# Kernel optimization log

Measured on AMD Instinct MI355X. Metric: run time of the kernel, lower is better.

Reference implementation:

```python
import jax, jax.numpy as jnp
import numpy as np

TOP_K = 2
NOISE_STD = 1.0
EPS = 1e-9

def setup_inputs() -> dict:
    key = jax.random.key(0)
    k1, k2, k3, k4 = jax.random.split(key, 4)
    B, S, H, E = 4, 4096, 4096, 64
    hidden_states = jax.random.normal(k1, (B, S, H), dtype=jnp.float32)
    noise = jax.random.normal(k2, (B, S, E), dtype=jnp.float32)
    lim = 1.0 / np.sqrt(H)  # torch Linear default init scale
    w_gate = jax.random.uniform(k3, (E, H), dtype=jnp.float32, minval=-lim, maxval=lim)
    w_noise = jax.random.uniform(k4, (E, H), dtype=jnp.float32, minval=-lim, maxval=lim)
    return {"hidden_states": hidden_states, "noise": noise, "w_gate": w_gate, "w_noise": w_noise}

def reference(hidden_states, noise, w_gate, w_noise):
    # Gate and noise projections: [B,S,H] x [E,H]^T -> [B,S,E]
    router_logits = jnp.einsum('bsh,eh->bse', hidden_states, w_gate)
    noise_scale = jax.nn.softplus(jnp.einsum('bsh,eh->bse', hidden_states, w_noise))
    router_logits = router_logits + noise * noise_scale * NOISE_STD
    router_probs = jax.nn.softmax(router_logits, axis=-1)
    top_k_weights, top_k_indices = jax.lax.top_k(router_probs, TOP_K)
    top_k_weights = top_k_weights / (jnp.sum(top_k_weights, axis=-1, keepdims=True) + EPS)
    # Scatter normalized weights back to dense [B,S,E] via one-hot (E is small)
    E = router_probs.shape[-1]
    gate_weights = jnp.sum(jax.nn.one_hot(top_k_indices, E, dtype=router_probs.dtype) * top_k_weights[..., None], axis=-2)
    return gate_weights, top_k_indices, router_logits
```

## Files before the change

kernel.cpp:

```cpp
#include <hip/hip_runtime.h>
#include <math.h>


typedef float   f32x4   __attribute__((ext_vector_type(4)));
typedef __bf16  bf16x8  __attribute__((ext_vector_type(8)));
typedef unsigned short ushort8 __attribute__((ext_vector_type(8)));

#define EE 64
#define E2 128
#define NT 8
#define BM 64

__device__ __forceinline__ unsigned short bf16_rne(float f) {
    unsigned int u = __float_as_uint(f);
    u += 0x7fffu + ((u >> 16) & 1u);
    return (unsigned short)(u >> 16);
}
__device__ __forceinline__ float bf16_f32(unsigned short h) {
    return __uint_as_float(((unsigned int)h) << 16);
}
__device__ __forceinline__ void split3(float a, unsigned short& h1,
                                       unsigned short& h2, unsigned short& h3) {
    h1 = bf16_rne(a);
    float r  = a - bf16_f32(h1);
    h2 = bf16_rne(r);
    float r2 = r - bf16_f32(h2);
    h3 = bf16_rne(r2);
}

__device__ __forceinline__ void gload_lds16(const void* g, void* l) {
    __builtin_amdgcn_global_load_lds(
        (const __attribute__((address_space(1))) void*)g,
        (__attribute__((address_space(3))) void*)l, 16, 0, 0);
}

__global__ __launch_bounds__(256) void pack_b(
    const float* __restrict__ wg, const float* __restrict__ wn,
    unsigned short* __restrict__ bp, int Hdim)
{
    int pair = blockIdx.x * 4 + (threadIdx.x >> 6);
    int l    = threadIdx.x & 63;
    int ks   = pair >> 3;
    int nt   = pair & 7;
    int col  = nt * 16 + (l & 15);
    int k    = ks * 32 + ((l >> 4) * 8);
    const float* wrow = (col < EE) ? (wg + (size_t)col * Hdim)
                                   : (wn + (size_t)(col - EE) * Hdim);
    float4 v0 = *reinterpret_cast<const float4*>(wrow + k);
    float4 v1 = *reinterpret_cast<const float4*>(wrow + k + 4);
    float vals[8] = {v0.x, v0.y, v0.z, v0.w, v1.x, v1.y, v1.z, v1.w};
    ushort8 t1, t2, t3;
    #pragma unroll
    for (int j = 0; j < 8; ++j) {
        unsigned short a, b, c;
        split3(vals[j], a, b, c);
        t1[j] = a; t2[j] = b; t3[j] = c;
    }
    size_t base = ((size_t)(ks * 8 + nt) * 3) * 512 + (size_t)l * 8;
    *reinterpret_cast<ushort8*>(bp + base        ) = t1;
    *reinterpret_cast<ushort8*>(bp + base + 512  ) = t2;
    *reinterpret_cast<ushort8*>(bp + base + 1024 ) = t3;
}

#define MFMA(a, b, c) __builtin_amdgcn_mfma_f32_16x16x32_bf16((a), (b), (c), 0, 0, 0)

__global__ __launch_bounds__(512, 2) void router_mfma(
    const float* __restrict__ hs,
    const float* __restrict__ noise,
    const unsigned short* __restrict__ bp,
    float* __restrict__ out_gate,
    float* __restrict__ out_idx,
    float* __restrict__ out_logits,
    int Ntok, int Hdim)
{
    __shared__ unsigned short Bst[2][2][24 * 512];
    __shared__ float Lred[BM][E2 + 5];

    const int tid  = threadIdx.x;
    const int lane = tid & 63;
    const int w    = tid >> 6;
    const int kh   = w >> 2;
    const int mi   = w & 3;
    const int m0   = blockIdx.x * BM;

    const int khalf = Hdim >> 1;
    const int steps = khalf >> 5;

    f32x4 acc[NT];
    #pragma unroll
    for (int nt = 0; nt < NT; ++nt) acc[nt] = f32x4{0.f, 0.f, 0.f, 0.f};

    const float* pa = hs + (size_t)(m0 + mi * 16 + (lane & 15)) * Hdim
                         + (size_t)kh * khalf + ((lane >> 4) * 8);

    const unsigned short* srcB[6];
    unsigned short* dstB[2][6];
    #pragma unroll
    for (int j = 0; j < 6; ++j) {
        int c   = tid + 512 * j;
        int ckh = c / 1536;
        int r   = c % 1536;
        int f   = r >> 6;
        int l   = r & 63;
        srcB[j]    = bp + (size_t)(ckh * steps) * 12288 + f * 512 + l * 8;
        dstB[0][j] = &Bst[0][ckh][f * 512 + l * 8];
        dstB[1][j] = &Bst[1][ckh][f * 512 + l * 8];
    }

    #define STAGE(buf)                                                        \
        do {                                                                  \
            _Pragma("unroll")                                                 \
            for (int j = 0; j < 6; ++j) {                                     \
                gload_lds16(srcB[j], dstB[buf][j]);                           \
                srcB[j] += 12288;                                             \
            }                                                                 \
        } while (0)

    #define LOADA(d0, d1)                                                     \
        do {                                                                  \
            d0 = *reinterpret_cast<const float4*>(pa);                        \
            d1 = *reinterpret_cast<const float4*>(pa + 4);                    \
            pa += 32;                                                         \
        } while (0)

    #define COMPUTE(s0, s1, buf)                                              \
        do {                                                                  \
            float vals[8] = {s0.x, s0.y, s0.z, s0.w, s1.x, s1.y, s1.z, s1.w}; \
            bf16x8 A1, A2, A3;                                                \
            _Pragma("unroll")                                                 \
            for (int j = 0; j < 8; ++j) {                                     \
                float a  = vals[j];                                           \
                __bf16 h1 = (__bf16)a;                                        \
                float r  = a - (float)h1;                                     \
                __bf16 h2 = (__bf16)r;                                        \
                float r2 = r - (float)h2;                                     \
                __bf16 h3 = (__bf16)r2;                                       \
                A1[j] = h1; A2[j] = h2; A3[j] = h3;                           \
            }                                                                 \
            const unsigned short* bb = &Bst[buf][kh][lane * 8];               \
            ushort8 bf[24];                                                   \
            _Pragma("unroll")                                                 \
            for (int f = 0; f < 24; ++f)                                      \
                bf[f] = *reinterpret_cast<const ushort8*>(bb + f * 512);      \
            _Pragma("unroll")                                                 \
            for (int nt = 0; nt < NT; ++nt) {                                 \
                bf16x8 b1 = __builtin_bit_cast(bf16x8, bf[nt * 3 + 0]);       \
                bf16x8 b2 = __builtin_bit_cast(bf16x8, bf[nt * 3 + 1]);       \
                bf16x8 b3 = __builtin_bit_cast(bf16x8, bf[nt * 3 + 2]);       \
                f32x4 c = acc[nt];                                            \
                c = MFMA(A1, b1, c);                                          \
                c = MFMA(A1, b2, c);                                          \
                c = MFMA(A2, b1, c);                                          \
                c = MFMA(A2, b2, c);                                          \
                c = MFMA(A1, b3, c);                                          \
                c = MFMA(A3, b1, c);                                          \
                acc[nt] = c;                                                  \
            }                                                                 \
        } while (0)

    STAGE(0);
    float4 c0, c1, n0, n1;
    LOADA(c0, c1);
    __syncthreads();

    for (int s = 0; s < steps; s += 2) {
        STAGE(1);
        LOADA(n0, n1);
        COMPUTE(c0, c1, 0);
        __syncthreads();
        if (s + 2 < steps) {
            STAGE(0);
            LOADA(c0, c1);
        }
        COMPUTE(n0, n1, 1);
        __syncthreads();
    }

    if (kh == 0) {
        #pragma unroll
        for (int nt = 0; nt < NT; ++nt)
            #pragma unroll
            for (int r = 0; r < 4; ++r)
                Lred[mi * 16 + (lane >> 4) * 4 + r][nt * 16 + (lane & 15)] = acc[nt][r];
    }
    __syncthreads();
    if (kh == 1) {
        #pragma unroll
        for (int nt = 0; nt < NT; ++nt)
            #pragma unroll
            for (int r = 0; r < 4; ++r)
                Lred[mi * 16 + (lane >> 4) * 4 + r][nt * 16 + (lane & 15)] += acc[nt][r];
    }
    __syncthreads();

    if (tid < BM) {
        const int t   = tid;
        const int tok = m0 + t;
        const float* nrow = noise + (size_t)tok * EE;
        float* lrow = out_logits + (size_t)tok * EE;

        float m = -3.4e38f;
        for (int e = 0; e < EE; ++e) {
            float gv = Lred[t][e];
            float nv = Lred[t][EE + e];
            float sp = fmaxf(nv, 0.f) + log1pf(expf(-fabsf(nv)));
            float l  = fmaf(nrow[e], sp, gv);
            lrow[e]  = l;
            Lred[t][e] = l;
            m = fmaxf(m, l);
        }

        float Z = 0.f;
        float p1 = -1.f, p2 = -1.f;
        int   i1 = 0,    i2 = 0;
        for (int e = 0; e < EE; ++e) {
            float p = expf(Lred[t][e] - m);
            Z += p;
            if (p > p1)      { p2 = p1; i2 = i1; p1 = p; i1 = e; }
            else if (p > p2) { p2 = p;  i2 = e; }
        }
        float q1 = p1 / Z, q2 = p2 / Z;
        float denom = q1 + q2 + 1e-9f;
        float w1 = q1 / denom, w2 = q2 / denom;

        out_idx[(size_t)tok * 2 + 0] = (float)i1;
        out_idx[(size_t)tok * 2 + 1] = (float)i2;

        float* grow = out_gate + (size_t)tok * EE;
        for (int e = 0; e < EE; ++e)
            grow[e] = (e == i1) ? w1 : ((e == i2) ? w2 : 0.f);
    }
}

extern "C" void kernel_launch(void* const* d_in, const int* in_sizes, int n_in,
                              void* d_out, int out_size, void* d_ws, size_t ws_size,
                              hipStream_t stream) {
    const float* hs    = (const float*)d_in[0];
    const float* noise = (const float*)d_in[1];
    const float* wg    = (const float*)d_in[2];
    const float* wn    = (const float*)d_in[3];

    const int Ntok = in_sizes[1] / EE;
    const int Hdim = in_sizes[2] / EE;

    float* out_gate   = (float*)d_out;
    float* out_idx    = out_gate + (size_t)Ntok * EE;
    float* out_logits = out_idx  + (size_t)Ntok * 2;

    unsigned short* bp = (unsigned short*)d_ws;

    int pairs = (Hdim / 32) * 8;
    hipLaunchKernelGGL(pack_b, dim3(pairs / 4), dim3(256), 0, stream, wg, wn, bp, Hdim);

    hipLaunchKernelGGL(router_mfma, dim3(Ntok / BM), dim3(512), 0, stream,
                       hs, noise, bp, out_gate, out_idx, out_logits, Ntok, Hdim);
}
```

Before: 161.8 us.

## Split expert columns across waves instead of K halves, shrink block tile

Changes the work split inside a block: rather than two K-halves each computing all 128 output columns for 64 rows, the block now takes 32 rows and each of 8 waves owns 16 rows by 32 columns across the full K range. This removes the cross-wave K reduction, cuts accumulator registers and LDS (Bst and Lred now share a union), and raises the occupancy target to 4 blocks per CU. It also wraps the MFMA sequence in s_setprio. The cost is that each wave now converts its A tile into three bf16 parts for a quarter of the MFMA work, so the split overhead per MFMA goes up, and since each block covers half as many rows, the B operand gets less reuse per LDS load.

Result: slower. 241.5 us (+49.2%).

```diff
diff --git a/kernel.cpp b/kernel.cpp
--- a/kernel.cpp
+++ b/kernel.cpp
@@ -8,8 +8,7 @@
 
 #define EE 64
 #define E2 128
-#define NT 8
-#define BM 64
+#define BM 32
 
 __device__ __forceinline__ unsigned short bf16_rne(float f) {
     unsigned int u = __float_as_uint(f);
@@ -64,7 +63,12 @@
 
 #define MFMA(a, b, c) __builtin_amdgcn_mfma_f32_16x16x32_bf16((a), (b), (c), 0, 0, 0)
 
-__global__ __launch_bounds__(512, 2) void router_mfma(
+union ShMem {
+    unsigned short Bst[2][24 * 512];
+    float Lred[BM][E2 + 5];
+};
+
+__global__ __launch_bounds__(512, 4) void router_mfma(
     const float* __restrict__ hs,
     const float* __restrict__ noise,
     const unsigned short* __restrict__ bp,
@@ -73,44 +77,39 @@
     float* __restrict__ out_logits,
     int Ntok, int Hdim)
 {
-    __shared__ unsigned short Bst[2][2][24 * 512];
-    __shared__ float Lred[BM][E2 + 5];
+    __shared__ ShMem sh;
 
     const int tid  = threadIdx.x;
     const int lane = tid & 63;
     const int w    = tid >> 6;
-    const int kh   = w >> 2;
-    const int mi   = w & 3;
+    const int mi   = w & 1;
+    const int nq   = w >> 1;
     const int m0   = blockIdx.x * BM;
 
-    const int khalf = Hdim >> 1;
-    const int steps = khalf >> 5;
-
-    f32x4 acc[NT];
+    const int steps = Hdim >> 5;
+
+    f32x4 acc0 = f32x4{0.f, 0.f, 0.f, 0.f};
+    f32x4 acc1 = f32x4{0.f, 0.f, 0.f, 0.f};
+
+    const float* pa = hs + (size_t)(m0 + mi * 16 + (lane & 15)) * Hdim
+                         + ((lane >> 4) * 8);
+
+    const unsigned short* srcB[3];
+    unsigned short* dstB[2][3];
     #pragma unroll
-    for (int nt = 0; nt < NT; ++nt) acc[nt] = f32x4{0.f, 0.f, 0.f, 0.f};
-
-    const float* pa = hs + (size_t)(m0 + mi * 16 + (lane & 15)) * Hdim
-                         + (size_t)kh * khalf + ((lane >> 4) * 8);
-
-    const unsigned short* srcB[6];
-    unsigned short* dstB[2][6];
-    #pragma unroll
-    for (int j = 0; j < 6; ++j) {
-        int c   = tid + 512 * j;
-        int ckh = c / 1536;
-        int r   = c % 1536;
-        int f   = r >> 6;
-        int l   = r & 63;
-        srcB[j]    = bp + (size_t)(ckh * steps) * 12288 + f * 512 + l * 8;
-        dstB[0][j] = &Bst[0][ckh][f * 512 + l * 8];
-        dstB[1][j] = &Bst[1][ckh][f * 512 + l * 8];
+    for (int j = 0; j < 3; ++j) {
+        int c = tid + 512 * j;
+        int f = c >> 6;
+        int l = c & 63;
+        srcB[j]    = bp + (size_t)f * 512 + l * 8;
+        dstB[0][j] = &sh.Bst[0][f * 512 + l * 8];
+        dstB[1][j] = &sh.Bst[1][f * 512 + l * 8];
     }
 
     #define STAGE(buf)                                                        \
         do {                                                                  \
             _Pragma("unroll")                                                 \
-            for (int j = 0; j < 6; ++j) {                                     \
+            for (int j = 0; j < 3; ++j) {                                     \
                 gload_lds16(srcB[j], dstB[buf][j]);                           \
                 srcB[j] += 12288;                                             \
             }                                                                 \
@@ -137,25 +136,27 @@
                 __bf16 h3 = (__bf16)r2;                                       \
                 A1[j] = h1; A2[j] = h2; A3[j] = h3;                           \
             }                                                                 \
-            const unsigned short* bb = &Bst[buf][kh][lane * 8];               \
-            ushort8 bf[24];                                                   \
-            _Pragma("unroll")                                                 \
-            for (int f = 0; f < 24; ++f)                                      \
-                bf[f] = *reinterpret_cast<const ushort8*>(bb + f * 512);      \
-            _Pragma("unroll")                                                 \
-            for (int nt = 0; nt < NT; ++nt) {                                 \
-                bf16x8 b1 = __builtin_bit_cast(bf16x8, bf[nt * 3 + 0]);       \
-                bf16x8 b2 = __builtin_bit_cast(bf16x8, bf[nt * 3 + 1]);       \
-                bf16x8 b3 = __builtin_bit_cast(bf16x8, bf[nt * 3 + 2]);       \
-                f32x4 c = acc[nt];                                            \
-                c = MFMA(A1, b1, c);                                          \
-                c = MFMA(A1, b2, c);                                          \
-                c = MFMA(A2, b1, c);                                          \
-                c = MFMA(A2, b2, c);                                          \
-                c = MFMA(A1, b3, c);                                          \
-                c = MFMA(A3, b1, c);                                          \
-                acc[nt] = c;                                                  \
-            }                                                                 \
+            const unsigned short* bb = &sh.Bst[buf][lane * 8];                \
+            bf16x8 b10 = __builtin_bit_cast(bf16x8, *reinterpret_cast<const ushort8*>(bb + (nq * 6 + 0) * 512)); \
+            bf16x8 b20 = __builtin_bit_cast(bf16x8, *reinterpret_cast<const ushort8*>(bb + (nq * 6 + 1) * 512)); \
+            bf16x8 b30 = __builtin_bit_cast(bf16x8, *reinterpret_cast<const ushort8*>(bb + (nq * 6 + 2) * 512)); \
+            bf16x8 b11 = __builtin_bit_cast(bf16x8, *reinterpret_cast<const ushort8*>(bb + (nq * 6 + 3) * 512)); \
+            bf16x8 b21 = __builtin_bit_cast(bf16x8, *reinterpret_cast<const ushort8*>(bb + (nq * 6 + 4) * 512)); \
+            bf16x8 b31 = __builtin_bit_cast(bf16x8, *reinterpret_cast<const ushort8*>(bb + (nq * 6 + 5) * 512)); \
+            __builtin_amdgcn_s_setprio(1);                                    \
+            acc0 = MFMA(A1, b10, acc0);                                       \
+            acc0 = MFMA(A1, b20, acc0);                                       \
+            acc0 = MFMA(A2, b10, acc0);                                       \
+            acc0 = MFMA(A2, b20, acc0);                                       \
+            acc0 = MFMA(A1, b30, acc0);                                       \
+            acc0 = MFMA(A3, b10, acc0);                                       \
+            acc1 = MFMA(A1, b11, acc1);                                       \
+            acc1 = MFMA(A1, b21, acc1);                                       \
+            acc1 = MFMA(A2, b11, acc1);                                       \
+            acc1 = MFMA(A2, b21, acc1);                                       \
+            acc1 = MFMA(A1, b31, acc1);                                       \
+            acc1 = MFMA(A3, b11, acc1);                                       \
+            __builtin_amdgcn_s_setprio(0);                                    \
         } while (0)
 
     STAGE(0);
@@ -176,20 +177,14 @@
         __syncthreads();
     }
 
-    if (kh == 0) {
+    {
+        int row = mi * 16 + (lane >> 4) * 4;
+        int col = nq * 32 + (lane & 15);
         #pragma unroll
-        for (int nt = 0; nt < NT; ++nt)
-            #pragma unroll
-            for (int r = 0; r < 4; ++r)
-                Lred[mi * 16 + (lane >> 4) * 4 + r][nt * 16 + (lane & 15)] = acc[nt][r];
-    }
-    __syncthreads();
-    if (kh == 1) {
-        #pragma unroll
-        for (int nt = 0; nt < NT; ++nt)
-            #pragma unroll
-            for (int r = 0; r < 4; ++r)
-                Lred[mi * 16 + (lane >> 4) * 4 + r][nt * 16 + (lane & 15)] += acc[nt][r];
+        for (int r = 0; r < 4; ++r) {
+            sh.Lred[row + r][col]      = acc0[r];
+            sh.Lred[row + r][col + 16] = acc1[r];
+        }
     }
     __syncthreads();
 
@@ -201,12 +196,12 @@
 
         float m = -3.4e38f;
         for (int e = 0; e < EE; ++e) {
-            float gv = Lred[t][e];
-            float nv = Lred[t][EE + e];
+            float gv = sh.Lred[t][e];
+            float nv = sh.Lred[t][EE + e];
             float sp = fmaxf(nv, 0.f) + log1pf(expf(-fabsf(nv)));
             float l  = fmaf(nrow[e], sp, gv);
             lrow[e]  = l;
-            Lred[t][e] = l;
+            sh.Lred[t][e] = l;
             m = fmaxf(m, l);
         }
 
@@ -214,7 +209,7 @@
         float p1 = -1.f, p2 = -1.f;
         int   i1 = 0,    i2 = 0;
         for (int e = 0; e < EE; ++e) {
-            float p = expf(Lred[t][e] - m);
+            float p = expf(sh.Lred[t][e] - m);
             Z += p;
             if (p > p1)      { p2 = p1; i2 = i1; p1 = p; i1 = e; }
             else if (p > p2) { p2 = p;  i2 = e; }
```
